# Kernel optimization log

Measured on AMD Instinct MI355X. Metric: run time of the kernel, lower is better.

Reference implementation:

```python
import jax, jax.numpy as jnp
import numpy as np
import math

EMB_DIM = 2048
HEAD_NUMS = 16
HEAD_DIM = EMB_DIM // HEAD_NUMS


def setup_inputs() -> dict:
    key = jax.random.key(0)
    k1, k2, k3, k4, k5 = jax.random.split(key, 5)
    B, S = 2, 2048
    X = jax.random.normal(k1, (B, S, EMB_DIM), dtype=jnp.float32)
    mask = jnp.ones((B, S), dtype=jnp.int32)
    # torch nn.Linear weights: [out_features, in_features]
    W_qkv = jax.random.normal(k2, (3 * EMB_DIM, EMB_DIM), dtype=jnp.float32) / math.sqrt(EMB_DIM)
    b_qkv = jax.random.normal(k3, (3 * EMB_DIM,), dtype=jnp.float32) * 0.01
    W_o = jax.random.normal(k4, (EMB_DIM, EMB_DIM), dtype=jnp.float32) / math.sqrt(EMB_DIM)
    b_o = jax.random.normal(k5, (EMB_DIM,), dtype=jnp.float32) * 0.01
    return {"X": X, "mask": mask, "W_qkv": W_qkv, "b_qkv": b_qkv, "W_o": W_o, "b_o": b_o}


def _rope_tables(seq_len):
    # Bug-faithful to source: exponent divides by full emb_dim, not head_dim.
    angle = 1.0 / jnp.power(10000.0, jnp.arange(0, HEAD_DIM, 2, dtype=jnp.float32) / EMB_DIM)
    t = jnp.arange(seq_len, dtype=jnp.float32)
    freqs = t[:, None] * angle[None, :]            # [S, HEAD_DIM//2]
    freqs = jnp.repeat(freqs, 2, axis=-1)          # [S, HEAD_DIM] (repeat_interleave)
    return jnp.cos(freqs), jnp.sin(freqs)


def _trans(x):
    # de-interleave pairs, then concat([-odd, even]) along last dim (as in source)
    B, H, S, D = x.shape
    xr = x.reshape(B, H, S, D // 2, 2)
    x1, x2 = xr[..., 0], xr[..., 1]
    return jnp.concatenate([-x2, x1], axis=-1)


def reference(X, mask, W_qkv, b_qkv, W_o, b_o):
    B, S, E = X.shape
    cos, sin = _rope_tables(S)                      # [S, HEAD_DIM]
    qkv = X @ W_qkv.T + b_qkv                       # [B, S, 3E]
    qkv = qkv.reshape(B, S, 3, HEAD_NUMS, HEAD_DIM).transpose(2, 0, 3, 1, 4)
    Q, K, V = qkv[0], qkv[1], qkv[2]                # [B, H, S, D]
    c = cos[None, None, :, :]
    s = sin[None, None, :, :]
    Q = c * Q + s * _trans(Q)
    K = c * K + s * _trans(K)
    scores = jnp.einsum('bhqd,bhkd->bhqk', Q, K) / math.sqrt(HEAD_DIM)
    pad = mask[:, None, None, :]                    # [B,1,1,S]
    scores = jnp.where(pad == 0, -1e9, scores)
    attn = jax.nn.softmax(scores, axis=-1)          # dropout = identity (eval)
    out = jnp.einsum('bhqk,bhkd->bhqd', attn, V)    # [B,H,S,D]
    out = out.transpose(0, 2, 1, 3).reshape(B, S, E)
    return out @ W_o.T + b_o
```

## Files before the change

kernel.cpp:

```cpp
#include <hip/hip_runtime.h>
#include <hip/hip_bf16.h>
#include <math.h>

typedef __bf16 bf16x8 __attribute__((ext_vector_type(8)));
typedef float  f32x4  __attribute__((ext_vector_type(4)));
typedef float  f32x16 __attribute__((ext_vector_type(16)));
typedef unsigned short ushort_t;
typedef ushort_t us4 __attribute__((ext_vector_type(4)));

#define MFMA16(a, b, c) __builtin_amdgcn_mfma_f32_16x16x32_bf16((a), (b), (c), 0, 0, 0)
#define MFMA32(a, b, c) __builtin_amdgcn_mfma_f32_32x32x16_bf16((a), (b), (c), 0, 0, 0)

__device__ __forceinline__ float bf2f(ushort_t h) {
    union { unsigned u; float f; } v; v.u = ((unsigned)h) << 16; return v.f;
}
__device__ __forceinline__ ushort_t f2bf(float x) {
    union { float f; unsigned u; } v; v.f = x;
    unsigned r = v.u + 0x7FFFu + ((v.u >> 16) & 1u);
    return (ushort_t)(r >> 16);
}
__device__ __forceinline__ void gl2lds16(const void* g, void* l) {
    __builtin_amdgcn_global_load_lds((__attribute__((address_space(1))) void*)(g),
                                     (__attribute__((address_space(3))) void*)(l),
                                     16, 0, 0);
}

__global__ __launch_bounds__(256) void detect_kernel(const ushort_t* __restrict__ w, int* flag)
{
    __shared__ int cnt[256];
    const int t = threadIdx.x;
    int c = 0;
    for (int i = t; i < 65536; i += 256) {
        const unsigned hw = w[i];
        const unsigned e = (hw >> 7) & 0xFFu;
        if (e == 0xFFu || (e == 0u && (hw & 0x7Fu) != 0u)) c++;
    }
    cnt[t] = c;
    __syncthreads();
    for (int s = 128; s > 0; s >>= 1) {
        if (t < s) cnt[t] += cnt[t + s];
        __syncthreads();
    }
    if (t == 0) flag[0] = (cnt[0] >= 8) ? 1 : 0;
}

__global__ __launch_bounds__(256) void convert_kernel(const void* __restrict__ src,
                                                      ushort_t* __restrict__ dst,
                                                      int n, const int* __restrict__ flag)
{
    const int i0 = (blockIdx.x * 256 + threadIdx.x) * 8;
    if (i0 + 8 > n) return;
    if (flag[0]) {
        const f32x4 a = *(const f32x4*)((const float*)src + i0);
        const f32x4 b = *(const f32x4*)((const float*)src + i0 + 4);
        ushort_t o[8];
        o[0]=f2bf(a[0]); o[1]=f2bf(a[1]); o[2]=f2bf(a[2]); o[3]=f2bf(a[3]);
        o[4]=f2bf(b[0]); o[5]=f2bf(b[1]); o[6]=f2bf(b[2]); o[7]=f2bf(b[3]);
        *(bf16x8*)(dst + i0) = *(const bf16x8*)o;
    } else {
        *(bf16x8*)(dst + i0) = *(const bf16x8*)((const ushort_t*)src + i0);
    }
}

__global__ __launch_bounds__(256) void gemm_bt_bias(
    const ushort_t* __restrict__ A, const ushort_t* __restrict__ B,
    const ushort_t* __restrict__ bias, ushort_t* __restrict__ C,
    int M, int N, int K)
{
    __shared__ __align__(16) ushort_t As[128 * 32];
    __shared__ __align__(16) ushort_t Bs[128 * 32];
    const int tid = threadIdx.x;
    const int w = tid >> 6, l = tid & 63, q = l >> 4, ln = l & 15;
    const int wm = w >> 1, wn = w & 1;
    const int m0 = blockIdx.y * 128, n0 = blockIdx.x * 128;
    const int sr = tid >> 2;
    const int sc = (tid & 3) * 8;

    f32x4 acc[4][4];
    const f32x4 z4 = {0.f, 0.f, 0.f, 0.f};
    for (int i = 0; i < 4; i++) for (int j = 0; j < 4; j++) acc[i][j] = z4;

    for (int k0 = 0; k0 < K; k0 += 32) {
        __syncthreads();
        gl2lds16(A + (size_t)(m0 + sr) * K + k0 + sc,       As + sr * 32 + sc);
        gl2lds16(A + (size_t)(m0 + 64 + sr) * K + k0 + sc,  As + (64 + sr) * 32 + sc);
        gl2lds16(B + (size_t)(n0 + sr) * K + k0 + sc,       Bs + sr * 32 + sc);
        gl2lds16(B + (size_t)(n0 + 64 + sr) * K + k0 + sc,  Bs + (64 + sr) * 32 + sc);
        __syncthreads();
        bf16x8 a[4], bb[4];
        for (int i = 0; i < 4; i++)
            a[i]  = *(const bf16x8*)(As + (wm * 64 + i * 16 + ln) * 32 + q * 8);
        for (int j = 0; j < 4; j++)
            bb[j] = *(const bf16x8*)(Bs + (wn * 64 + j * 16 + ln) * 32 + q * 8);
        for (int i = 0; i < 4; i++)
            for (int j = 0; j < 4; j++)
                acc[i][j] = MFMA16(a[i], bb[j], acc[i][j]);
    }
    for (int j = 0; j < 4; j++) {
        const int n = n0 + wn * 64 + j * 16 + ln;
        const float bv = bf2f(bias[n]);
        for (int i = 0; i < 4; i++) {
            const int mrow = m0 + wm * 64 + i * 16 + q * 4;
            for (int r = 0; r < 4; r++)
                C[(size_t)(mrow + r) * N + n] = f2bf(acc[i][j][r] + bv);
        }
    }
}

__global__ __launch_bounds__(256) void gemm_bt_bias_out(
    const ushort_t* __restrict__ A, const ushort_t* __restrict__ B,
    const ushort_t* __restrict__ bias, void* __restrict__ C,
    int M, int N, int K, const int* __restrict__ flag)
{
    __shared__ __align__(16) ushort_t As[128 * 32];
    __shared__ __align__(16) ushort_t Bs[128 * 32];
    const int tid = threadIdx.x;
    const int w = tid >> 6, l = tid & 63, q = l >> 4, ln = l & 15;
    const int wm = w >> 1, wn = w & 1;
    const int m0 = blockIdx.y * 128, n0 = blockIdx.x * 128;
    const int sr = tid >> 2;
    const int sc = (tid & 3) * 8;

    f32x4 acc[4][4];
    const f32x4 z4 = {0.f, 0.f, 0.f, 0.f};
    for (int i = 0; i < 4; i++) for (int j = 0; j < 4; j++) acc[i][j] = z4;

    for (int k0 = 0; k0 < K; k0 += 32) {
        __syncthreads();
        gl2lds16(A + (size_t)(m0 + sr) * K + k0 + sc,       As + sr * 32 + sc);
        gl2lds16(A + (size_t)(m0 + 64 + sr) * K + k0 + sc,  As + (64 + sr) * 32 + sc);
        gl2lds16(B + (size_t)(n0 + sr) * K + k0 + sc,       Bs + sr * 32 + sc);
        gl2lds16(B + (size_t)(n0 + 64 + sr) * K + k0 + sc,  Bs + (64 + sr) * 32 + sc);
        __syncthreads();
        bf16x8 a[4], bb[4];
        for (int i = 0; i < 4; i++)
            a[i]  = *(const bf16x8*)(As + (wm * 64 + i * 16 + ln) * 32 + q * 8);
        for (int j = 0; j < 4; j++)
            bb[j] = *(const bf16x8*)(Bs + (wn * 64 + j * 16 + ln) * 32 + q * 8);
        for (int i = 0; i < 4; i++)
            for (int j = 0; j < 4; j++)
                acc[i][j] = MFMA16(a[i], bb[j], acc[i][j]);
    }
    const int f = flag[0];
    for (int j = 0; j < 4; j++) {
        const int n = n0 + wn * 64 + j * 16 + ln;
        const float bv = bf2f(bias[n]);
        for (int i = 0; i < 4; i++) {
            const int mrow = m0 + wm * 64 + i * 16 + q * 4;
            for (int r = 0; r < 4; r++) {
                const float val = acc[i][j][r] + bv;
                const size_t idx = (size_t)(mrow + r) * N + n;
                if (f) ((float*)C)[idx] = val;
                else   ((ushort_t*)C)[idx] = f2bf(val);
            }
        }
    }
}

__global__ __launch_bounds__(256) void rope_kernel(ushort_t* qkv)
{
    const int bs = blockIdx.x;
    const int s = bs & 2047;
    const int t = threadIdx.x;
    const size_t base = (size_t)bs * 6144;
    float cv[8], sv[8], qa[8], qp[8], ka[8], kp[8];
    for (int u = 0; u < 8; u++) {
        const int e = u * 256 + t;
        const int j = e & 127;
        const int p = (j < 64) ? (2 * j + 1) : (2 * (j - 64));
        const int hb = e - j;
        const float ang = powf(10000.0f, -(float)(2 * (j >> 1)) / 2048.0f);
        sincosf((float)s * ang, &sv[u], &cv[u]);
        qa[u] = bf2f(qkv[base + hb + j]);
        qp[u] = bf2f(qkv[base + hb + p]);
        ka[u] = bf2f(qkv[base + 2048 + hb + j]);
        kp[u] = bf2f(qkv[base + 2048 + hb + p]);
    }
    __syncthreads();
    for (int u = 0; u < 8; u++) {
        const int e = u * 256 + t;
        const int j = e & 127;
        const int hb = e - j;
        const float sg = (j < 64) ? -1.0f : 1.0f;
        qkv[base + hb + j]        = f2bf(cv[u] * qa[u] + sv[u] * sg * qp[u]);
        qkv[base + 2048 + hb + j] = f2bf(cv[u] * ka[u] + sv[u] * sg * kp[u]);
    }
}

__global__ __launch_bounds__(256) void vtrans_kernel(const ushort_t* __restrict__ qkv,
                                                     ushort_t* __restrict__ Vt)
{
    __shared__ ushort_t tile[64][130];
    const int blk = blockIdx.x;
    const int st = blk & 31, h = (blk >> 5) & 15, b = blk >> 9;
    const int t = threadIdx.x;
    for (int i = 0; i < 32; i++) {
        const int e = i * 256 + t;
        const int r = e >> 7, c = e & 127;
        tile[r][c] = qkv[(size_t)(b * 2048 + st * 64 + r) * 6144 + 4096 + h * 128 + c];
    }
    __syncthreads();
    const int d = t >> 1, s0 = (t & 1) * 32;
    const size_t obase = ((size_t)(b * 16 + h) * 128 + d) * 2048 + st * 64 + s0;
    for (int k = 0; k < 32; k++)
        Vt[obase + k] = tile[s0 + k][d];
}

__global__ __launch_bounds__(256) void flash_kernel(
    const ushort_t* __restrict__ qkv, const ushort_t* __restrict__ Vt,
    const int* __restrict__ mask, ushort_t* __restrict__ AO)
{
    __shared__ __align__(16) ushort_t Ks[64 * 136];
    __shared__ __align__(16) ushort_t Vs[128 * 136];
    __shared__ __align__(16) ushort_t Ps[4 * 32 * 72];
    const int t = threadIdx.x;
    const int w = t >> 6, l = t & 63, lq = l & 31, q2 = l >> 5;
    const int qb = blockIdx.x * 128, h = blockIdx.y, b = blockIdx.z;
    const size_t brow = (size_t)b * 2048;
    const float scale = 0.08838834764831845f;
    const int qrow = qb + w * 32 + lq;

    bf16x8 qf[8];
#pragma unroll
    for (int kb = 0; kb < 8; kb++)
        qf[kb] = *(const bf16x8*)(qkv + (brow + qrow) * 6144 + h * 128 + kb * 16 + q2 * 8);

    float m_old = -1e30f, lsum = 0.f;
    f32x16 acc_o[4];
#pragma unroll
    for (int dt = 0; dt < 4; dt++)
#pragma unroll
        for (int r = 0; r < 16; r++) acc_o[dt][r] = 0.f;

    for (int s0 = 0; s0 < 2048; s0 += 64) {
        const int mk = mask[brow + s0 + l];
        const unsigned long long bm = __ballot(mk != 0);
        __syncthreads();
#pragma unroll
        for (int i = 0; i < 4; i++) {
            const int c = i * 256 + t;
            const int row = c >> 4, cb = c & 15;
            *(bf16x8*)(Ks + row * 136 + cb * 8) =
                *(const bf16x8*)(qkv + (brow + s0 + row) * 6144 + 2048 + h * 128 + cb * 8);
        }
#pragma unroll
        for (int i = 0; i < 4; i++) {
            const int c = i * 256 + t;
            const int row = c >> 3, cb = c & 7;
            *(bf16x8*)(Vs + row * 136 + cb * 8) =
                *(const bf16x8*)(Vt + ((size_t)(b * 16 + h) * 128 + row) * 2048 + s0 + cb * 8);
        }
        __syncthreads();
        f32x16 sa[2];
#pragma unroll
        for (int mt = 0; mt < 2; mt++) {
#pragma unroll
            for (int r = 0; r < 16; r++) sa[mt][r] = 0.f;
#pragma unroll
            for (int kb = 0; kb < 8; kb++) {
                bf16x8 a = *(const bf16x8*)(Ks + (mt * 32 + lq) * 136 + kb * 16 + q2 * 8);
                sa[mt] = MFMA32(a, qf[kb], sa[mt]);
            }
        }
        float p[32];
        float mr = -1e30f;
#pragma unroll
        for (int mt = 0; mt < 2; mt++)
#pragma unroll
            for (int r = 0; r < 16; r++) {
                const int srow = mt * 32 + (r & 3) + 8 * (r >> 2) + 4 * q2;
                const float bias = ((bm >> srow) & 1ull) ? 0.f : -1e9f;
                const float v = sa[mt][r] * scale + bias;
                p[mt * 16 + r] = v;
                mr = fmaxf(mr, v);
            }
        mr = fmaxf(mr, __shfl_xor(mr, 32, 64));
        const float mnew = fmaxf(m_old, mr);
        const float alpha = __expf(m_old - mnew);
        float rs = 0.f;
#pragma unroll
        for (int i = 0; i < 32; i++) { p[i] = __expf(p[i] - mnew); rs += p[i]; }
        rs += __shfl_xor(rs, 32, 64);
        lsum = alpha * lsum + rs;
        m_old = mnew;
#pragma unroll
        for (int dt = 0; dt < 4; dt++)
#pragma unroll
            for (int r = 0; r < 16; r++) acc_o[dt][r] *= alpha;
#pragma unroll
        for (int mt = 0; mt < 2; mt++)
#pragma unroll
            for (int r2 = 0; r2 < 4; r2++) {
                us4 pk;
#pragma unroll
                for (int j = 0; j < 4; j++) pk[j] = f2bf(p[mt * 16 + r2 * 4 + j]);
                *(us4*)(Ps + (w * 32 + lq) * 72 + mt * 32 + r2 * 8 + q2 * 4) = pk;
            }
        bf16x8 pf[4];
#pragma unroll
        for (int kb = 0; kb < 4; kb++)
            pf[kb] = *(const bf16x8*)(Ps + (w * 32 + lq) * 72 + kb * 16 + q2 * 8);
#pragma unroll
        for (int dt = 0; dt < 4; dt++)
#pragma unroll
            for (int kb = 0; kb < 4; kb++) {
                bf16x8 va = *(const bf16x8*)(Vs + (dt * 32 + lq) * 136 + kb * 16 + q2 * 8);
                acc_o[dt] = MFMA32(va, pf[kb], acc_o[dt]);
            }
    }
    __syncthreads();
    const float inv = (lsum > 0.f) ? 1.0f / lsum : 0.f;
#pragma unroll
    for (int dt = 0; dt < 4; dt++)
#pragma unroll
        for (int r2 = 0; r2 < 4; r2++) {
            us4 ov;
#pragma unroll
            for (int j = 0; j < 4; j++) ov[j] = f2bf(acc_o[dt][r2 * 4 + j] * inv);
            *(us4*)(Vs + (w * 32 + lq) * 136 + dt * 32 + r2 * 8 + q2 * 4) = ov;
        }
#pragma unroll
    for (int i = 0; i < 8; i++) {
        const int row = i * 4 + (l >> 4), ch = l & 15;
        bf16x8 vv = *(const bf16x8*)(Vs + (w * 32 + row) * 136 + ch * 8);
        *(bf16x8*)(AO + (brow + qb + w * 32 + row) * 2048 + h * 128 + ch * 8) = vv;
    }
}

extern "C" void kernel_launch(void* const* d_in, const int* in_sizes, int n_in,
                              void* d_out, int out_size, void* d_ws, size_t ws_size,
                              hipStream_t stream)
{
    (void)in_sizes; (void)n_in; (void)out_size; (void)ws_size;
    const void* X    = d_in[0];
    const int*  mask = (const int*)d_in[1];
    const void* Wqkv = d_in[2];
    const void* bqkv = d_in[3];
    const void* Wo   = d_in[4];
    const void* bo   = d_in[5];

    int*      flag  = (int*)d_ws;
    ushort_t* Xc    = (ushort_t*)d_ws + 16;
    ushort_t* Wqkvc = Xc + 8388608;
    ushort_t* bqkvc = Wqkvc + 12582912;
    ushort_t* Woc   = bqkvc + 6144;
    ushort_t* boc   = Woc + 4194304;
    ushort_t* qkv   = boc + 2048;
    ushort_t* Vt    = Wqkvc;
    ushort_t* AO    = Xc;

    detect_kernel<<<1, 256, 0, stream>>>((const ushort_t*)Wqkv, flag);
    convert_kernel<<<4096, 256, 0, stream>>>(X,    Xc,    8388608,  flag);
    convert_kernel<<<6144, 256, 0, stream>>>(Wqkv, Wqkvc, 12582912, flag);
    convert_kernel<<<3,    256, 0, stream>>>(bqkv, bqkvc, 6144,     flag);
    convert_kernel<<<2048, 256, 0, stream>>>(Wo,   Woc,   4194304,  flag);
    convert_kernel<<<1,    256, 0, stream>>>(bo,   boc,   2048,     flag);

    gemm_bt_bias<<<dim3(6144 / 128, 4096 / 128), 256, 0, stream>>>(Xc, Wqkvc, bqkvc, qkv, 4096, 6144, 2048);
    rope_kernel<<<4096, 256, 0, stream>>>(qkv);
    vtrans_kernel<<<1024, 256, 0, stream>>>(qkv, Vt);
    flash_kernel<<<dim3(16, 16, 2), 256, 0, stream>>>(qkv, Vt, mask, AO);
    gemm_bt_bias_out<<<dim3(2048 / 128, 4096 / 128), 256, 0, stream>>>(AO, Woc, boc, d_out, 4096, 2048, 2048, flag);
}
```

Measured before the change: 655.6 us.

## Replace QKV projection GEMM with 256x256-tile, 8-wave, multi-stage pipelined kernel

Swaps the 128x128, single-buffered QKV GEMM for a 256x256-tile kernel with 512 threads and a 4-slot LDS ring covering two K-steps of 32. Global-to-LDS loads for the next step are interleaved with MFMA phases, and explicit vmcnt waits, raw barriers and setprio are used. An XOR swizzle on LDS rows reduces bank conflicts. The goal is to hide load latency and raise arithmetic intensity, at the cost of 128KB of LDS per block, more registers, and a grid of only 384 blocks.

```diff
diff --git a/kernel.cpp b/kernel.cpp
--- a/kernel.cpp
+++ b/kernel.cpp
@@ -62,49 +62,171 @@
     }
 }
 
-__global__ __launch_bounds__(256) void gemm_bt_bias(
+__global__ __launch_bounds__(512, 2) void gemm256_bt_bias(
     const ushort_t* __restrict__ A, const ushort_t* __restrict__ B,
     const ushort_t* __restrict__ bias, ushort_t* __restrict__ C,
     int M, int N, int K)
 {
-    __shared__ __align__(16) ushort_t As[128 * 32];
-    __shared__ __align__(16) ushort_t Bs[128 * 32];
+    __shared__ __align__(16) ushort_t SM[65536];
     const int tid = threadIdx.x;
-    const int w = tid >> 6, l = tid & 63, q = l >> 4, ln = l & 15;
-    const int wm = w >> 1, wn = w & 1;
-    const int m0 = blockIdx.y * 128, n0 = blockIdx.x * 128;
-    const int sr = tid >> 2;
-    const int sc = (tid & 3) * 8;
-
-    f32x4 acc[4][4];
+    const int l = tid & 63, ln = l & 15, q2 = l >> 4;
+    const int w = tid >> 6, wm = w >> 2, wn = w & 3;
+    const int m0 = blockIdx.y * 256, n0 = blockIdx.x * 256;
+    const int NT = K >> 6;
+
+#define STG_A256(slot, kbase, o) do { \
+    const int s_ = (o) * 512 + tid; const int r_ = s_ >> 2; \
+    const int q_ = (s_ & 3) ^ ((r_ >> 1) & 3); \
+    gl2lds16(A + (size_t)(m0 + r_) * K + (kbase) + q_ * 8, \
+             SM + (slot) * 16384 + s_ * 8); } while (0)
+#define STG_B256(slot, kbase, o) do { \
+    const int s_ = (o) * 512 + tid; const int r_ = s_ >> 2; \
+    const int q_ = (s_ & 3) ^ ((r_ >> 1) & 3); \
+    gl2lds16(B + (size_t)(n0 + r_) * K + (kbase) + q_ * 8, \
+             SM + (slot) * 16384 + 8192 + s_ * 8); } while (0)
+#define DSA256(slot, row) (*(const bf16x8*)(SM + (slot) * 16384 + (row) * 32 + ((q2 ^ (((row) >> 1) & 3)) << 3)))
+#define DSB256(slot, row) (*(const bf16x8*)(SM + (slot) * 16384 + 8192 + (row) * 32 + ((q2 ^ (((row) >> 1) & 3)) << 3)))
+#define BAR256() asm volatile("s_barrier" ::: "memory")
+
+    f32x4 acc[8][4];
     const f32x4 z4 = {0.f, 0.f, 0.f, 0.f};
-    for (int i = 0; i < 4; i++) for (int j = 0; j < 4; j++) acc[i][j] = z4;
-
-    for (int k0 = 0; k0 < K; k0 += 32) {
-        __syncthreads();
-        gl2lds16(A + (size_t)(m0 + sr) * K + k0 + sc,       As + sr * 32 + sc);
-        gl2lds16(A + (size_t)(m0 + 64 + sr) * K + k0 + sc,  As + (64 + sr) * 32 + sc);
-        gl2lds16(B + (size_t)(n0 + sr) * K + k0 + sc,       Bs + sr * 32 + sc);
-        gl2lds16(B + (size_t)(n0 + 64 + sr) * K + k0 + sc,  Bs + (64 + sr) * 32 + sc);
-        __syncthreads();
-        bf16x8 a[4], bb[4];
-        for (int i = 0; i < 4; i++)
-            a[i]  = *(const bf16x8*)(As + (wm * 64 + i * 16 + ln) * 32 + q * 8);
-        for (int j = 0; j < 4; j++)
-            bb[j] = *(const bf16x8*)(Bs + (wn * 64 + j * 16 + ln) * 32 + q * 8);
-        for (int i = 0; i < 4; i++)
-            for (int j = 0; j < 4; j++)
-                acc[i][j] = MFMA16(a[i], bb[j], acc[i][j]);
-    }
+#pragma unroll
+    for (int i = 0; i < 8; i++)
+#pragma unroll
+        for (int j = 0; j < 4; j++) acc[i][j] = z4;
+
+    STG_A256(0, 0, 0);  STG_A256(0, 0, 1);  STG_B256(0, 0, 0);  STG_B256(0, 0, 1);
+    STG_A256(1, 32, 0); STG_A256(1, 32, 1); STG_B256(1, 32, 0); STG_B256(1, 32, 1);
+    if (NT > 1) STG_A256(2, 64, 0);
+    asm volatile("s_waitcnt vmcnt(5)" ::: "memory");
+    BAR256();
+
+    for (int t = 0; t < NT; ++t) {
+        const int s0 = (2 * t) & 3, s1 = (2 * t + 1) & 3;
+        const int sA = (2 * t + 2) & 3, sB = (2 * t + 3) & 3;
+        const int kA = (t + 1) << 6, kB = kA + 32, kC = (t + 2) << 6;
+        const bool stAB = (t < NT - 1), stC = (t < NT - 2);
+        const int rA0 = wm * 128, rA1 = wm * 128 + 64, rB = wn * 64;
+        bf16x8 a0[4], a1[4], b00[2], b01[2], b10[2], b11[2];
+
+#pragma unroll
+        for (int ii = 0; ii < 4; ii++) a0[ii] = DSA256(s0, rA0 + ii * 16 + ln);
+        b00[0] = DSB256(s0, rB + ln);
+        b00[1] = DSB256(s0, rB + 16 + ln);
+        if (stAB) STG_A256(sA, kA, 1);
+        __builtin_amdgcn_s_setprio(1);
+#pragma unroll
+        for (int ii = 0; ii < 4; ii++) {
+            acc[ii][0] = MFMA16(a0[ii], b00[0], acc[ii][0]);
+            acc[ii][1] = MFMA16(a0[ii], b00[1], acc[ii][1]);
+        }
+        __builtin_amdgcn_s_setprio(0);
+        if (stAB) { asm volatile("s_waitcnt vmcnt(2)" ::: "memory"); }
+        else      { asm volatile("s_waitcnt vmcnt(0)" ::: "memory"); }
+        BAR256();
+
+#pragma unroll
+        for (int ii = 0; ii < 4; ii++) a1[ii] = DSA256(s1, rA0 + ii * 16 + ln);
+        b01[0] = DSB256(s1, rB + ln);
+        b01[1] = DSB256(s1, rB + 16 + ln);
+        if (stAB) STG_B256(sA, kA, 0);
+        __builtin_amdgcn_s_setprio(1);
+#pragma unroll
+        for (int ii = 0; ii < 4; ii++) {
+            acc[ii][0] = MFMA16(a1[ii], b01[0], acc[ii][0]);
+            acc[ii][1] = MFMA16(a1[ii], b01[1], acc[ii][1]);
+        }
+        __builtin_amdgcn_s_setprio(0);
+        BAR256();
+
+        b10[0] = DSB256(s0, rB + 32 + ln);
+        b10[1] = DSB256(s0, rB + 48 + ln);
+        if (stAB) STG_B256(sA, kA, 1);
+        __builtin_amdgcn_s_setprio(1);
+#pragma unroll
+        for (int ii = 0; ii < 4; ii++) {
+            acc[ii][2] = MFMA16(a0[ii], b10[0], acc[ii][2]);
+            acc[ii][3] = MFMA16(a0[ii], b10[1], acc[ii][3]);
+        }
+        __builtin_amdgcn_s_setprio(0);
+        BAR256();
+
+        b11[0] = DSB256(s1, rB + 32 + ln);
+        b11[1] = DSB256(s1, rB + 48 + ln);
+        if (stAB) STG_A256(sB, kB, 0);
+        __builtin_amdgcn_s_setprio(1);
+#pragma unroll
+        for (int ii = 0; ii < 4; ii++) {
+            acc[ii][2] = MFMA16(a1[ii], b11[0], acc[ii][2]);
+            acc[ii][3] = MFMA16(a1[ii], b11[1], acc[ii][3]);
+        }
+        __builtin_amdgcn_s_setprio(0);
+        BAR256();
+
+#pragma unroll
+        for (int ii = 0; ii < 4; ii++) a0[ii] = DSA256(s0, rA1 + ii * 16 + ln);
+        if (stAB) STG_A256(sB, kB, 1);
+        __builtin_amdgcn_s_setprio(1);
+#pragma unroll
+        for (int ii = 0; ii < 4; ii++) {
+            acc[4 + ii][2] = MFMA16(a0[ii], b10[0], acc[4 + ii][2]);
+            acc[4 + ii][3] = MFMA16(a0[ii], b10[1], acc[4 + ii][3]);
+        }
+        __builtin_amdgcn_s_setprio(0);
+        BAR256();
+
+#pragma unroll
+        for (int ii = 0; ii < 4; ii++) a1[ii] = DSA256(s1, rA1 + ii * 16 + ln);
+        if (stAB) STG_B256(sB, kB, 0);
+        __builtin_amdgcn_s_setprio(1);
+#pragma unroll
+        for (int ii = 0; ii < 4; ii++) {
+            acc[4 + ii][2] = MFMA16(a1[ii], b11[0], acc[4 + ii][2]);
+            acc[4 + ii][3] = MFMA16(a1[ii], b11[1], acc[4 + ii][3]);
+        }
+        __builtin_amdgcn_s_setprio(0);
+        BAR256();
+
+        if (stAB) STG_B256(sB, kB, 1);
+        __builtin_amdgcn_s_setprio(1);
+#pragma unroll
+        for (int ii = 0; ii < 4; ii++) {
+            acc[4 + ii][0] = MFMA16(a0[ii], b00[0], acc[4 + ii][0]);
+            acc[4 + ii][1] = MFMA16(a0[ii], b00[1], acc[4 + ii][1]);
+        }
+        __builtin_amdgcn_s_setprio(0);
+        BAR256();
+
+        if (stC) STG_A256(s0, kC, 0);
+        __builtin_amdgcn_s_setprio(1);
+#pragma unroll
+        for (int ii = 0; ii < 4; ii++) {
+            acc[4 + ii][0] = MFMA16(a1[ii], b01[0], acc[4 + ii][0]);
+            acc[4 + ii][1] = MFMA16(a1[ii], b01[1], acc[4 + ii][1]);
+        }
+        __builtin_amdgcn_s_setprio(0);
+        if (t < NT - 2)       { asm volatile("s_waitcnt vmcnt(5)" ::: "memory"); }
+        else if (t == NT - 2) { asm volatile("s_waitcnt vmcnt(4)" ::: "memory"); }
+        BAR256();
+    }
+
+#pragma unroll
     for (int j = 0; j < 4; j++) {
         const int n = n0 + wn * 64 + j * 16 + ln;
         const float bv = bf2f(bias[n]);
-        for (int i = 0; i < 4; i++) {
-            const int mrow = m0 + wm * 64 + i * 16 + q * 4;
+#pragma unroll
+        for (int i = 0; i < 8; i++) {
+            const int mrow = m0 + wm * 128 + i * 16 + q2 * 4;
+#pragma unroll
             for (int r = 0; r < 4; r++)
                 C[(size_t)(mrow + r) * N + n] = f2bf(acc[i][j][r] + bv);
         }
     }
+#undef STG_A256
+#undef STG_B256
+#undef DSA256
+#undef DSB256
+#undef BAR256
 }
 
 __global__ __launch_bounds__(256) void gemm_bt_bias_out(
@@ -356,7 +478,7 @@
     convert_kernel<<<2048, 256, 0, stream>>>(Wo,   Woc,   4194304,  flag);
     convert_kernel<<<1,    256, 0, stream>>>(bo,   boc,   2048,     flag);
 
-    gemm_bt_bias<<<dim3(6144 / 128, 4096 / 128), 256, 0, stream>>>(Xc, Wqkvc, bqkvc, qkv, 4096, 6144, 2048);
+    gemm256_bt_bias<<<dim3(6144 / 256, 4096 / 256), 512, 0, stream>>>(Xc, Wqkvc, bqkvc, qkv, 4096, 6144, 2048);
     rope_kernel<<<4096, 256, 0, stream>>>(qkv);
     vtrans_kernel<<<1024, 256, 0, stream>>>(qkv, Vt);
     flash_kernel<<<dim3(16, 16, 2), 256, 0, stream>>>(qkv, Vt, mask, AO);
```

Result: faster. 608.9 us (-7.1%).
